# Performance work log

Measured on AMD Instinct MI355X. Metric: run time of the kernel, lower is better.

The kernel has to match this reference:

```python
import jax, jax.numpy as jnp
import numpy as np

NUM_ROUNDS = 4

def leaky(x):
    return jnp.where(x >= 0, x, 0.01 * x)  # nn.LeakyReLU default slope

def setup_inputs() -> dict:
    key = jax.random.key(0)
    ks = jax.random.split(key, 26)
    N, E2, B = 50000, 320000, 256
    Fn, Fe, D, Dn, Dx, H, NE = 64, 16, 128, 128, 16, 128, 8
    # edges come in reverse pairs so edge i and edge rev[i] are (u->v) and (v->u)
    s = jax.random.randint(ks[0], (E2,), 0, N, dtype=jnp.int32)
    d = jax.random.randint(ks[1], (E2,), 0, N, dtype=jnp.int32)
    src = jnp.concatenate([s, d])
    dst = jnp.concatenate([d, s])
    rev = jnp.concatenate([jnp.arange(E2, dtype=jnp.int32) + E2,
                           jnp.arange(E2, dtype=jnp.int32)])
    gid = jnp.sort(jax.random.randint(ks[2], (N,), 0, B, dtype=jnp.int32))
    r = lambda k, sh: (jax.random.normal(k, sh, jnp.float32) * 0.1)
    Fin = Dn + Dx  # MoE input feature size
    return {
        'node_feat': r(ks[3], (N, Fn)),
        'edge_feat': r(ks[4], (2 * E2, Fe)),
        'src': src, 'dst': dst, 'rev': rev, 'gid': gid,
        'extra': r(ks[5], (B, Dx)),
        'W_edge': r(ks[6], (Fn + Fe, D)),
        'W_upd': r(ks[7], (D, D)),
        'W_node': r(ks[8], (Fn + D, Dn)), 'b_node': r(ks[9], (Dn,)),
        'Wg1': r(ks[10], (Fin, H)), 'bg1': r(ks[11], (H,)),
        'Wg2': r(ks[12], (H, H)), 'bg2': r(ks[13], (H,)),
        'Wg3': r(ks[14], (H, NE)), 'bg3': r(ks[15], (NE,)),
        'EW1': r(ks[16], (NE, Fin, H)), 'Eb1': r(ks[17], (NE, H)),
        'EW2': r(ks[18], (NE, H, H)), 'Eb2': r(ks[19], (NE, H)),
        'EW3': r(ks[20], (NE, H)), 'Eb3': r(ks[21], (NE,)),
    }

def reference(node_feat, edge_feat, src, dst, rev, gid, extra,
              W_edge, W_upd, W_node, b_node,
              Wg1, bg1, Wg2, bg2, Wg3, bg3,
              EW1, Eb1, EW2, Eb2, EW3, Eb3):
    N = node_feat.shape[0]
    B = extra.shape[0]
    # h0 = edge_mlp(cat(src node feat, edge feat)) ; dropout = identity (eval)
    h0 = leaky(jnp.concatenate([node_feat[src], edge_feat], axis=1) @ W_edge)  # [E, D]
    h = h0
    for _ in range(NUM_ROUNDS):
        sum0 = jax.ops.segment_sum(h, dst, num_segments=N)       # incoming sum per node
        m = sum0[src] - h[rev]                                   # exclude reverse message
        h = leaky(m @ W_upd + h0)
    m_node = jax.ops.segment_sum(h, dst, num_segments=N)         # [N, D]
    hn = leaky(jnp.concatenate([node_feat, m_node], axis=1) @ W_node + b_node)  # [N, Dn]
    # NOTE: original computes multi-head attention on hn.unsqueeze(1) but discards it.
    graph_feat = jax.ops.segment_sum(hn, gid, num_segments=B)    # readout sum [B, Dn]
    x = jnp.concatenate([graph_feat, extra], axis=-1)            # [B, Fin]
    # gating
    g = leaky(x @ Wg1 + bg1)
    g = leaky(g @ Wg2 + bg2)
    g = jax.nn.softmax(g @ Wg3 + bg3, axis=1)                    # [B, NE]
    # experts (vectorized over expert dim)
    e = leaky(jnp.einsum('bi,eih->beh', x, EW1) + Eb1)
    e = leaky(jnp.einsum('beh,ehk->bek', e, EW2) + Eb2)
    e = jnp.einsum('beh,eh->be', e, EW3) + Eb3                   # [B, NE]
    return jnp.sum(e * g, axis=1, keepdims=True)                 # [B, 1]
```

## Files before the change

kernel.cpp:

```cpp
#include <hip/hip_runtime.h>
#include <stdint.h>
#include <stddef.h>


typedef unsigned short u16;
typedef u16 u16x2 __attribute__((ext_vector_type(2)));
typedef u16 u16x4 __attribute__((ext_vector_type(4)));
typedef u16 u16x8 __attribute__((ext_vector_type(8)));
typedef short s16x8 __attribute__((ext_vector_type(8)));
typedef float f32x4_ __attribute__((ext_vector_type(4)));

__device__ __forceinline__ float lk(float x) { return x >= 0.f ? x : 0.01f * x; }

__device__ __forceinline__ float bf2f(u16 u) {
    union { uint32_t i; float f; } v; v.i = ((uint32_t)u) << 16; return v.f;
}
__device__ __forceinline__ u16 f2bf(float f) {
    union { float f; uint32_t i; } v; v.f = f;
    uint32_t r = v.i + 0x7FFFu + ((v.i >> 16) & 1u);
    return (u16)(r >> 16);
}

__global__ void k_zero_i32(int* __restrict__ p, int n) {
    int i = blockIdx.x * blockDim.x + threadIdx.x;
    if (i < n) p[i] = 0;
}
__global__ void k_zero_f32(float* __restrict__ p, int n) {
    int i = blockIdx.x * blockDim.x + threadIdx.x;
    if (i < n) p[i] = 0.f;
}

__global__ void k_prep_wu(const float* __restrict__ W, u16* __restrict__ wTg) {
    int i = blockIdx.x * 256 + threadIdx.x;
    if (i < 128 * 128) { int n = i >> 7, k = i & 127; wTg[i] = f2bf(W[k * 128 + n]); }
}
__global__ void k_prep_we(const float* __restrict__ W, u16* __restrict__ weTg) {
    int i = blockIdx.x * 256 + threadIdx.x;
    if (i < 128 * 96) {
        int n = i / 96, k = i - n * 96;
        weTg[i] = (k < 80) ? f2bf(W[k * 128 + n]) : (u16)0;
    }
}

__global__ void k_count(const int* __restrict__ dst, int* __restrict__ counts, int E) {
    int i = blockIdx.x * blockDim.x + threadIdx.x;
    if (i < E) atomicAdd(&counts[dst[i]], 1);
}

__global__ __launch_bounds__(1024) void k_scan(const int* __restrict__ counts,
                                               int* __restrict__ off, int Nn) {
    __shared__ int buf[1024];
    __shared__ int carry_s;
    int t = threadIdx.x;
    if (t == 0) carry_s = 0;
    __syncthreads();
    for (int base = 0; base < Nn; base += 8192) {
        int v[8]; int s = 0;
#pragma unroll
        for (int i = 0; i < 8; ++i) {
            int idx = base + t * 8 + i;
            v[i] = (idx < Nn) ? counts[idx] : 0;
            s += v[i];
        }
        int x = s;
        for (int o = 1; o < 1024; o <<= 1) {
            buf[t] = x; __syncthreads();
            if (t >= o) x += buf[t - o];
            __syncthreads();
        }
        int excl = carry_s + x - s;
#pragma unroll
        for (int i = 0; i < 8; ++i) {
            int idx = base + t * 8 + i;
            if (idx < Nn) off[idx] = excl;
            excl += v[i];
        }
        __syncthreads();
        if (t == 1023) carry_s += x;
        __syncthreads();
    }
    if (t == 0) off[Nn] = carry_s;
}

__global__ void k_fill(const int* __restrict__ dst, const int* __restrict__ off,
                       int* __restrict__ cursor, int* __restrict__ eidx, int E) {
    int i = blockIdx.x * blockDim.x + threadIdx.x;
    if (i < E) {
        int d = dst[i];
        int p = atomicAdd(&cursor[d], 1);
        eidx[off[d] + p] = i;
    }
}

__global__ __launch_bounds__(256) void k_segsum(const u16* __restrict__ h,
                                                const int* __restrict__ off,
                                                const int* __restrict__ eidx,
                                                float* __restrict__ out, int Nn) {
    int wid = threadIdx.x >> 6;
    int lane = threadIdx.x & 63;
    int n = blockIdx.x * 4 + wid;
    if (n >= Nn) return;
    int lo = off[n], hi = off[n + 1];
    float ax = 0.f, ay = 0.f;
    int j = lo;
    for (; j + 3 < hi; j += 4) {
        int ea = eidx[j], eb = eidx[j + 1], ec = eidx[j + 2], ed = eidx[j + 3];
        u16x2 va = *(const u16x2*)(h + (size_t)ea * 128 + lane * 2);
        u16x2 vb = *(const u16x2*)(h + (size_t)eb * 128 + lane * 2);
        u16x2 vc = *(const u16x2*)(h + (size_t)ec * 128 + lane * 2);
        u16x2 vd = *(const u16x2*)(h + (size_t)ed * 128 + lane * 2);
        ax += (bf2f(va[0]) + bf2f(vb[0])) + (bf2f(vc[0]) + bf2f(vd[0]));
        ay += (bf2f(va[1]) + bf2f(vb[1])) + (bf2f(vc[1]) + bf2f(vd[1]));
    }
    for (; j < hi; ++j) {
        int ea = eidx[j];
        u16x2 va = *(const u16x2*)(h + (size_t)ea * 128 + lane * 2);
        ax += bf2f(va[0]); ay += bf2f(va[1]);
    }
    float2 r; r.x = ax; r.y = ay;
    *(float2*)(out + (size_t)n * 128 + lane * 2) = r;
}


__global__ __launch_bounds__(256) void k_edge_init_mfma(
    const float* __restrict__ node_feat, const float* __restrict__ edge_feat,
    const int* __restrict__ src, const u16* __restrict__ weTg,
    u16* __restrict__ h) {
    __shared__ u16 x0[64][104];
    __shared__ u16 wTe[128][104];
    const int t = threadIdx.x;
    const int e0 = blockIdx.x * 64;
    {
        int n = t >> 1, half = t & 1;
        const u16* gsrc = weTg + n * 96 + half * 48;
        u16* ldst = &wTe[n][half * 48];
#pragma unroll
        for (int i = 0; i < 6; ++i)
            *(u16x8*)(ldst + i * 8) = *(const u16x8*)(gsrc + i * 8);
    }
    {
        int rloc = t & 63, part = t >> 6;
        int e = e0 + rloc;
        int s = src[e];
        const float* nf = node_feat + (size_t)s * 64;
        const float* ef = edge_feat + (size_t)e * 16;
#pragma unroll
        for (int i = 0; i < 5; ++i) {
            int f = part * 20 + i * 4;
            float4 v;
            if (f < 64) v = *(const float4*)(nf + f);
            else        v = *(const float4*)(ef + (f - 64));
            u16x4 o; o[0] = f2bf(v.x); o[1] = f2bf(v.y); o[2] = f2bf(v.z); o[3] = f2bf(v.w);
            *(u16x4*)(&x0[rloc][f]) = o;
        }
    }
    {
        int rr = t >> 2, part = t & 3;
        u16x4 z = {0, 0, 0, 0};
        *(u16x4*)(&x0[rr][80 + part * 4]) = z;
    }
    __syncthreads();
    const int w = t >> 6, l = t & 63;
    const int er = l & 15, kg = l >> 4;
    f32x4_ acc[8];
#pragma unroll
    for (int nt = 0; nt < 8; ++nt) { f32x4_ z = {0.f, 0.f, 0.f, 0.f}; acc[nt] = z; }
#pragma unroll
    for (int ks = 0; ks < 3; ++ks) {
        s16x8 bfrag = *(const s16x8*)(&x0[w * 16 + er][ks * 32 + kg * 8]);
#pragma unroll
        for (int nt = 0; nt < 8; ++nt) {
            s16x8 afrag = *(const s16x8*)(&wTe[nt * 16 + er][ks * 32 + kg * 8]);
            acc[nt] = __builtin_amdgcn_mfma_f32_16x16x32_bf16(afrag, bfrag, acc[nt], 0, 0, 0);
        }
    }
    {
        size_t gedge = (size_t)(e0 + w * 16 + er);
        u16* hr = h + gedge * 128;
#pragma unroll
        for (int nt = 0; nt < 8; ++nt) {
            int nc = nt * 16 + kg * 4;
            u16x4 o;
#pragma unroll
            for (int r = 0; r < 4; ++r) o[r] = f2bf(lk(acc[nt][r]));
            *(u16x4*)(hr + nc) = o;
        }
    }
}

__global__ __launch_bounds__(256) void k_update_mfma_recomp(
    u16* __restrict__ h, const float* __restrict__ sum0,
    const int* __restrict__ src, const int* __restrict__ rev,
    const u16* __restrict__ wTg, const u16* __restrict__ weTg,
    const float* __restrict__ node_feat, const float* __restrict__ edge_feat) {
    __shared__ __align__(16) u16 smem[64 * 136 + 128 * 136];
    __shared__ int eid[64];
    u16 (*x0)[104]  = (u16(*)[104])smem;
    u16 (*wTe)[104] = (u16(*)[104])(smem + 64 * 104);
    u16 (*mw)[136]  = (u16(*)[136])smem;
    u16 (*wT)[136]  = (u16(*)[136])(smem + 64 * 136);
    const int t = threadIdx.x;
    const int p0 = blockIdx.x * 32;
    const int w = t >> 6, l = t & 63;
    const int er = l & 15, kg = l >> 4;

    {
        int n = t >> 1, half = t & 1;
        const u16* gsrc = weTg + n * 96 + half * 48;
        u16* ldst = &wTe[n][half * 48];
#pragma unroll
        for (int i = 0; i < 6; ++i)
            *(u16x8*)(ldst + i * 8) = *(const u16x8*)(gsrc + i * 8);
    }
    {
        int rloc = t & 63, part = t >> 6;
        int gedge = (rloc < 32) ? (p0 + rloc) : rev[p0 + rloc - 32];
        if (part == 0) eid[rloc] = gedge;
        int s = src[gedge];
        const float* nf = node_feat + (size_t)s * 64;
        const float* ef = edge_feat + (size_t)gedge * 16;
#pragma unroll
        for (int i = 0; i < 5; ++i) {
            int f = part * 20 + i * 4;
            float4 v;
            if (f < 64) v = *(const float4*)(nf + f);
            else        v = *(const float4*)(ef + (f - 64));
            u16x4 o; o[0] = f2bf(v.x); o[1] = f2bf(v.y); o[2] = f2bf(v.z); o[3] = f2bf(v.w);
            *(u16x4*)(&x0[rloc][f]) = o;
        }
    }
    {
        int rr = t >> 2, part = t & 3;
        u16x4 z = {0, 0, 0, 0};
        *(u16x4*)(&x0[rr][80 + part * 4]) = z;
    }
    __syncthreads();

    f32x4_ acc[8];
#pragma unroll
    for (int nt = 0; nt < 8; ++nt) { f32x4_ z = {0.f, 0.f, 0.f, 0.f}; acc[nt] = z; }
#pragma unroll
    for (int ks = 0; ks < 3; ++ks) {
        s16x8 bfrag = *(const s16x8*)(&x0[w * 16 + er][ks * 32 + kg * 8]);
#pragma unroll
        for (int nt = 0; nt < 8; ++nt) {
            s16x8 afrag = *(const s16x8*)(&wTe[nt * 16 + er][ks * 32 + kg * 8]);
            acc[nt] = __builtin_amdgcn_mfma_f32_16x16x32_bf16(afrag, bfrag, acc[nt], 0, 0, 0);
        }
    }
    float h0reg[8][4];
#pragma unroll
    for (int nt = 0; nt < 8; ++nt)
#pragma unroll
        for (int r = 0; r < 4; ++r) h0reg[nt][r] = lk(acc[nt][r]);
    __syncthreads();

    {
        int wr = t >> 1, half = t & 1;
        const u16* gsrc = wTg + wr * 128 + half * 64;
        u16* ldst = &wT[wr][half * 64];
#pragma unroll
        for (int i = 0; i < 8; ++i)
            *(u16x8*)(ldst + i * 8) = *(const u16x8*)(gsrc + i * 8);
    }
    {
        int rr = t >> 2, part = t & 3;
        int gedge, partner;
        if (rr < 32) { gedge = p0 + rr;        partner = rev[gedge]; }
        else         { partner = p0 + rr - 32; gedge = rev[partner]; }
        int s = src[gedge];
        const float* sp = sum0 + (size_t)s * 128 + part * 32;
        const u16* hp = h + (size_t)partner * 128 + part * 32;
#pragma unroll
        for (int i = 0; i < 4; ++i) {
            float4 a0 = *(const float4*)(sp + i * 8);
            float4 a1 = *(const float4*)(sp + i * 8 + 4);
            u16x8 b = *(const u16x8*)(hp + i * 8);
            u16x8 o;
            o[0] = f2bf(a0.x - bf2f(b[0]));
            o[1] = f2bf(a0.y - bf2f(b[1]));
            o[2] = f2bf(a0.z - bf2f(b[2]));
            o[3] = f2bf(a0.w - bf2f(b[3]));
            o[4] = f2bf(a1.x - bf2f(b[4]));
            o[5] = f2bf(a1.y - bf2f(b[5]));
            o[6] = f2bf(a1.z - bf2f(b[6]));
            o[7] = f2bf(a1.w - bf2f(b[7]));
            *(u16x8*)(&mw[rr][part * 32 + i * 8]) = o;
        }
    }
    __syncthreads();

#pragma unroll
    for (int nt = 0; nt < 8; ++nt) { f32x4_ z = {0.f, 0.f, 0.f, 0.f}; acc[nt] = z; }
#pragma unroll
    for (int ks = 0; ks < 4; ++ks) {
        s16x8 bfrag = *(const s16x8*)(&mw[w * 16 + er][ks * 32 + kg * 8]);
#pragma unroll
        for (int nt = 0; nt < 8; ++nt) {
            s16x8 afrag = *(const s16x8*)(&wT[nt * 16 + er][ks * 32 + kg * 8]);
            acc[nt] = __builtin_amdgcn_mfma_f32_16x16x32_bf16(afrag, bfrag, acc[nt], 0, 0, 0);
        }
    }
    {
        int gedge = eid[w * 16 + er];
        u16* hr = h + (size_t)gedge * 128;
#pragma unroll
        for (int nt = 0; nt < 8; ++nt) {
            int nc = nt * 16 + kg * 4;
            u16x4 o;
#pragma unroll
            for (int r = 0; r < 4; ++r) o[r] = f2bf(lk(acc[nt][r] + h0reg[nt][r]));
            *(u16x4*)(hr + nc) = o;
        }
    }
}

#define KROW(i, m)                                                                 \
    acc[i][0] = fmaf(m, w0.x, acc[i][0]); acc[i][1] = fmaf(m, w0.y, acc[i][1]);    \
    acc[i][2] = fmaf(m, w0.z, acc[i][2]); acc[i][3] = fmaf(m, w0.w, acc[i][3]);    \
    acc[i][4] = fmaf(m, w1.x, acc[i][4]); acc[i][5] = fmaf(m, w1.y, acc[i][5]);    \
    acc[i][6] = fmaf(m, w1.z, acc[i][6]); acc[i][7] = fmaf(m, w1.w, acc[i][7]);

#define KSTEP(ARR, kk, kabs)                                                       \
    {                                                                              \
        const float m0 = ARR[et4 + 0][kabs];                                       \
        const float m1 = ARR[et4 + 1][kabs];                                       \
        const float m2 = ARR[et4 + 2][kabs];                                       \
        const float m3 = ARR[et4 + 3][kabs];                                       \
        const float4 w0 = *(const float4*)(&w_lds[(kk) * 128 + ct8]);              \
        const float4 w1 = *(const float4*)(&w_lds[(kk) * 128 + ct8 + 4]);          \
        KROW(0, m0) KROW(1, m1) KROW(2, m2) KROW(3, m3)                            \
    }

__global__ __launch_bounds__(256) void k_node(const float* __restrict__ node_feat,
                                              const float* __restrict__ m_node,
                                              const float* __restrict__ W,
                                              const float* __restrict__ bias,
                                              float* __restrict__ hn, int Nn) {
    __shared__ float in_lds[64][196];
    __shared__ float w_lds[16 * 128];
    const int t = threadIdx.x;
    const int n0 = blockIdx.x * 64;
    {
        int q = t & 31, r0 = t >> 5;
#pragma unroll
        for (int rr = r0; rr < 64; rr += 8) {
            int n = n0 + rr;
            bool ok = n < Nn;
            const float* nf = node_feat + (size_t)n * 64;
            const float* mn = m_node + (size_t)n * 128;
            for (int qq = q; qq < 48; qq += 32) {
                float4 v; v.x = v.y = v.z = v.w = 0.f;
                if (ok) {
                    if (qq < 16) v = *(const float4*)(nf + qq * 4);
                    else         v = *(const float4*)(mn + (qq - 16) * 4);
                }
                *(float4*)(&in_lds[rr][qq * 4]) = v;
            }
        }
    }
    float acc[4][8];
#pragma unroll
    for (int i = 0; i < 4; ++i)
#pragma unroll
        for (int j = 0; j < 8; ++j) acc[i][j] = 0.f;
    const int et4 = (t >> 4) * 4;
    const int ct8 = (t & 15) * 8;
    for (int kc = 0; kc < 192; kc += 16) {
        __syncthreads();
#pragma unroll
        for (int i = 0; i < 2; ++i) {
            int f4 = t + i * 256;
            *(float4*)(&w_lds[f4 * 4]) = *(const float4*)(W + (size_t)kc * 128 + (size_t)f4 * 4);
        }
        __syncthreads();
#pragma unroll 8
        for (int k = 0; k < 16; ++k) { KSTEP(in_lds, k, kc + k) }
    }
    float4 b0 = *(const float4*)(bias + ct8);
    float4 b1 = *(const float4*)(bias + ct8 + 4);
    __syncthreads();
#pragma unroll
    for (int i = 0; i < 4; ++i) {
        int row = n0 + et4 + i;
        if (row >= Nn) break;
        size_t base = (size_t)row * 128 + ct8;
        float4 o0, o1;
        o0.x = lk(acc[i][0] + b0.x); o0.y = lk(acc[i][1] + b0.y);
        o0.z = lk(acc[i][2] + b0.z); o0.w = lk(acc[i][3] + b0.w);
        o1.x = lk(acc[i][4] + b1.x); o1.y = lk(acc[i][5] + b1.y);
        o1.z = lk(acc[i][6] + b1.z); o1.w = lk(acc[i][7] + b1.w);
        *(float4*)(hn + base) = o0;
        *(float4*)(hn + base + 4) = o1;
    }
}

__device__ __forceinline__ int lbound(const int* __restrict__ a, int n, int key) {
    int lo = 0, hi = n;
    while (lo < hi) { int mid = (lo + hi) >> 1; if (a[mid] < key) lo = mid + 1; else hi = mid; }
    return lo;
}

__global__ __launch_bounds__(256) void k_readout(const float* __restrict__ hn,
                                                 const int* __restrict__ gid,
                                                 const float* __restrict__ extra,
                                                 float* __restrict__ x, int Nn) {
    int b = blockIdx.x;
    int t = threadIdx.x;
    int lo = lbound(gid, Nn, b);
    int hi = lbound(gid, Nn, b + 1);
    if (t < 128) {
        float acc = 0.f;
        int n = lo;
        for (; n + 3 < hi; n += 4) {
            acc += hn[(size_t)n * 128 + t] + hn[(size_t)(n + 1) * 128 + t]
                 + hn[(size_t)(n + 2) * 128 + t] + hn[(size_t)(n + 3) * 128 + t];
        }
        for (; n < hi; ++n) acc += hn[(size_t)n * 128 + t];
        x[(size_t)b * 144 + t] = acc;
    } else if (t < 144) {
        x[(size_t)b * 144 + t] = extra[(size_t)b * 16 + (t - 128)];
    }
}

__global__ __launch_bounds__(256) void k_moe(const float* __restrict__ x,
                                             const float* __restrict__ Wg1, const float* __restrict__ bg1,
                                             const float* __restrict__ Wg2, const float* __restrict__ bg2,
                                             const float* __restrict__ Wg3, const float* __restrict__ bg3,
                                             const float* __restrict__ EW1, const float* __restrict__ Eb1,
                                             const float* __restrict__ EW2, const float* __restrict__ Eb2,
                                             const float* __restrict__ EW3, const float* __restrict__ Eb3,
                                             float* __restrict__ out) {
    __shared__ float xs[144];
    __shared__ float g1s[128], g2s[128];
    __shared__ float e1s[8 * 128], e2s[8 * 128];
    __shared__ float logit_s[8], val_s[8];
    const int b = blockIdx.x;
    const int t = threadIdx.x;
    if (t < 144) xs[t] = x[(size_t)b * 144 + t];
    __syncthreads();
    if (t < 128) {
        float a = bg1[t];
        for (int k = 0; k < 144; ++k) a = fmaf(xs[k], Wg1[k * 128 + t], a);
        g1s[t] = lk(a);
    }
#pragma unroll
    for (int u = 0; u < 4; ++u) {
        int idx = t + u * 256;
        int e = idx >> 7, c = idx & 127;
        float a = Eb1[e * 128 + c];
        const float* w = EW1 + (size_t)e * 144 * 128 + c;
        for (int k = 0; k < 144; ++k) a = fmaf(xs[k], w[(size_t)k * 128], a);
        e1s[idx] = lk(a);
    }
    __syncthreads();
    if (t < 128) {
        float a = bg2[t];
        for (int k = 0; k < 128; ++k) a = fmaf(g1s[k], Wg2[k * 128 + t], a);
        g2s[t] = lk(a);
    }
#pragma unroll
    for (int u = 0; u < 4; ++u) {
        int idx = t + u * 256;
        int e = idx >> 7, c = idx & 127;
        float a = Eb2[e * 128 + c];
        const float* w = EW2 + (size_t)e * 128 * 128 + c;
        const float* e1p = e1s + e * 128;
        for (int k = 0; k < 128; ++k) a = fmaf(e1p[k], w[(size_t)k * 128], a);
        e2s[idx] = lk(a);
    }
    __syncthreads();
    if (t < 8) {
        float a = bg3[t];
        for (int k = 0; k < 128; ++k) a = fmaf(g2s[k], Wg3[k * 8 + t], a);
        logit_s[t] = a;
        float v = Eb3[t];
        const float* w = EW3 + t * 128;
        const float* ep = e2s + t * 128;
        for (int k = 0; k < 128; ++k) v = fmaf(ep[k], w[k], v);
        val_s[t] = v;
    }
    __syncthreads();
    if (t == 0) {
        float mx = logit_s[0];
        for (int e = 1; e < 8; ++e) mx = fmaxf(mx, logit_s[e]);
        float s = 0.f, o = 0.f;
        for (int e = 0; e < 8; ++e) {
            float g = __expf(logit_s[e] - mx);
            s += g;
            o = fmaf(val_s[e], g, o);
        }
        out[b] = o / s;
    }
}

extern "C" void kernel_launch(void* const* d_in, const int* in_sizes, int n_in,
                              void* d_out, int out_size, void* d_ws, size_t ws_size,
                              hipStream_t stream) {
    const float* node_feat = (const float*)d_in[0];
    const float* edge_feat = (const float*)d_in[1];
    const int*   src       = (const int*)d_in[2];
    const int*   dst       = (const int*)d_in[3];
    const int*   rev       = (const int*)d_in[4];
    const int*   gid       = (const int*)d_in[5];
    const float* extra     = (const float*)d_in[6];
    const float* W_edge    = (const float*)d_in[7];
    const float* W_upd     = (const float*)d_in[8];
    const float* W_node    = (const float*)d_in[9];
    const float* b_node    = (const float*)d_in[10];

    const int Nn = in_sizes[0] / 64;
    const int E  = in_sizes[2];
    const int Bb = in_sizes[6] / 16;
    (void)n_in;
    float* out = (float*)d_out;

    uintptr_t p = (uintptr_t)d_ws;
    auto alloc = [&](size_t bytes) -> void* {
        void* r = (void*)p;
        p += (bytes + 255) & ~(size_t)255;
        return r;
    };
    auto al = [](size_t b) { return (b + 255) & ~(size_t)255; };
    const size_t SHb = al((size_t)E * 128 * 2);
    const size_t fixed = al((size_t)Nn * 128 * 4) + al((size_t)Bb * 144 * 4) +
                         al((size_t)(Nn + 1) * 4) + al((size_t)(2 * Nn) * 4) +
                         al((size_t)E * 4) + al(128 * 128 * 2) + al(128 * 96 * 2) + 4096;
    const size_t need = SHb + fixed;

    if (ws_size < need) {
        k_zero_f32<<<(out_size + 255) / 256, 256, 0, stream>>>(out, out_size);
        return;
    }

    u16* h      = (u16*)alloc(SHb);
    float* sum0 = (float*)alloc((size_t)Nn * 128 * sizeof(float));
    float* xbuf = (float*)alloc((size_t)Bb * 144 * sizeof(float));
    int* off    = (int*)alloc((size_t)(Nn + 1) * sizeof(int));
    int* cc     = (int*)alloc((size_t)(2 * Nn) * sizeof(int));
    int* eidx   = (int*)alloc((size_t)E * sizeof(int));
    u16* wTg    = (u16*)alloc(128 * 128 * sizeof(u16));
    u16* weTg   = (u16*)alloc(128 * 96 * sizeof(u16));
    int* counts = cc;
    int* cursor = cc + Nn;

    k_zero_i32<<<(2 * Nn + 255) / 256, 256, 0, stream>>>(cc, 2 * Nn);

    const int csr_grid = (E + 255) / 256;
    k_count<<<csr_grid, 256, 0, stream>>>(dst, counts, E);
    k_scan<<<1, 1024, 0, stream>>>(counts, off, Nn);
    k_fill<<<csr_grid, 256, 0, stream>>>(dst, off, cursor, eidx, E);

    k_prep_wu<<<64, 256, 0, stream>>>(W_upd, wTg);
    k_prep_we<<<48, 256, 0, stream>>>(W_edge, weTg);

    const int egrid = E / 64;
    const int pgrid = (E / 2) / 32;
    const int sgrid = (Nn + 3) / 4;

    k_edge_init_mfma<<<egrid, 256, 0, stream>>>(node_feat, edge_feat, src, weTg, h);
    for (int r = 0; r < 4; ++r) {
        k_segsum<<<sgrid, 256, 0, stream>>>(h, off, eidx, sum0, Nn);
        k_update_mfma_recomp<<<pgrid, 256, 0, stream>>>(h, sum0, src, rev, wTg, weTg,
                                                        node_feat, edge_feat);
    }
    k_segsum<<<sgrid, 256, 0, stream>>>(h, off, eidx, sum0, Nn);

    float* hn = sum0;
    k_node<<<(Nn + 63) / 64, 256, 0, stream>>>(node_feat, sum0, W_node, b_node, hn, Nn);
    k_readout<<<Bb, 256, 0, stream>>>(hn, gid, extra, xbuf, Nn);
    k_moe<<<Bb, 256, 0, stream>>>(xbuf,
                                  (const float*)d_in[11], (const float*)d_in[12],
                                  (const float*)d_in[13], (const float*)d_in[14],
                                  (const float*)d_in[15], (const float*)d_in[16],
                                  (const float*)d_in[17], (const float*)d_in[18],
                                  (const float*)d_in[19], (const float*)d_in[20],
                                  (const float*)d_in[21], (const float*)d_in[22],
                                  out);
}
```

Baseline: 1.580 ms.

## Fuse segment sums into edge kernels via atomics and swizzle shared tiles

The edge-init and update kernels now scatter each bf16-rounded output row into a double-buffered per-node fp32 sum with atomicAdd. This removes the CSR build and the separate segment-sum gather passes when the workspace is large enough. The weight fragments are read straight from global memory instead of being staged in LDS, and the activation tile uses an XOR-swizzled layout in a smaller shared buffer, which raises occupancy. The cost is heavy atomic traffic (about 640k×128 float atomics per round), non-deterministic summation order, and an extra zeroing pass per round.

```diff
diff --git a/kernel.cpp b/kernel.cpp
--- a/kernel.cpp
+++ b/kernel.cpp
@@ -19,6 +19,10 @@
     union { float f; uint32_t i; } v; v.f = f;
     uint32_t r = v.i + 0x7FFFu + ((v.i >> 16) & 1u);
     return (u16)(r >> 16);
+}
+
+__device__ __forceinline__ int swz(int row, int k) {
+    return row * 128 + (k ^ ((row & 7) << 3));
 }
 
 __global__ void k_zero_i32(int* __restrict__ p, int n) {
@@ -122,22 +126,17 @@
 }
 
 
-__global__ __launch_bounds__(256) void k_edge_init_mfma(
+template <bool ATOMIC>
+__global__ __launch_bounds__(256) void k_edge_init_v2(
     const float* __restrict__ node_feat, const float* __restrict__ edge_feat,
-    const int* __restrict__ src, const u16* __restrict__ weTg,
-    u16* __restrict__ h) {
-    __shared__ u16 x0[64][104];
-    __shared__ u16 wTe[128][104];
+    const int* __restrict__ src, const int* __restrict__ dst,
+    const u16* __restrict__ weTg, u16* __restrict__ h,
+    float* __restrict__ sumAcc) {
+    __shared__ u16 tile[64 * 128];
     const int t = threadIdx.x;
     const int e0 = blockIdx.x * 64;
-    {
-        int n = t >> 1, half = t & 1;
-        const u16* gsrc = weTg + n * 96 + half * 48;
-        u16* ldst = &wTe[n][half * 48];
-#pragma unroll
-        for (int i = 0; i < 6; ++i)
-            *(u16x8*)(ldst + i * 8) = *(const u16x8*)(gsrc + i * 8);
-    }
+    const int w = t >> 6, l = t & 63;
+    const int er = l & 15, kg = l >> 4;
     {
         int rloc = t & 63, part = t >> 6;
         int e = e0 + rloc;
@@ -151,32 +150,32 @@
             if (f < 64) v = *(const float4*)(nf + f);
             else        v = *(const float4*)(ef + (f - 64));
             u16x4 o; o[0] = f2bf(v.x); o[1] = f2bf(v.y); o[2] = f2bf(v.z); o[3] = f2bf(v.w);
-            *(u16x4*)(&x0[rloc][f]) = o;
+            *(u16x4*)(&tile[swz(rloc, f)]) = o;
         }
     }
     {
         int rr = t >> 2, part = t & 3;
         u16x4 z = {0, 0, 0, 0};
-        *(u16x4*)(&x0[rr][80 + part * 4]) = z;
-    }
-    __syncthreads();
-    const int w = t >> 6, l = t & 63;
-    const int er = l & 15, kg = l >> 4;
+        *(u16x4*)(&tile[swz(rr, 80 + part * 4)]) = z;
+    }
+    __syncthreads();
     f32x4_ acc[8];
 #pragma unroll
     for (int nt = 0; nt < 8; ++nt) { f32x4_ z = {0.f, 0.f, 0.f, 0.f}; acc[nt] = z; }
 #pragma unroll
     for (int ks = 0; ks < 3; ++ks) {
-        s16x8 bfrag = *(const s16x8*)(&x0[w * 16 + er][ks * 32 + kg * 8]);
+        s16x8 bfrag = *(const s16x8*)(&tile[swz(w * 16 + er, ks * 32 + kg * 8)]);
 #pragma unroll
         for (int nt = 0; nt < 8; ++nt) {
-            s16x8 afrag = *(const s16x8*)(&wTe[nt * 16 + er][ks * 32 + kg * 8]);
+            s16x8 afrag = *(const s16x8*)(weTg + (nt * 16 + er) * 96 + ks * 32 + kg * 8);
             acc[nt] = __builtin_amdgcn_mfma_f32_16x16x32_bf16(afrag, bfrag, acc[nt], 0, 0, 0);
         }
     }
     {
-        size_t gedge = (size_t)(e0 + w * 16 + er);
-        u16* hr = h + gedge * 128;
+        int gedge = e0 + w * 16 + er;
+        u16* hr = h + (size_t)gedge * 128;
+        float* sr = nullptr;
+        if (ATOMIC) sr = sumAcc + (size_t)dst[gedge] * 128;
 #pragma unroll
         for (int nt = 0; nt < 8; ++nt) {
             int nc = nt * 16 + kg * 4;
@@ -184,38 +183,37 @@
 #pragma unroll
             for (int r = 0; r < 4; ++r) o[r] = f2bf(lk(acc[nt][r]));
             *(u16x4*)(hr + nc) = o;
-        }
-    }
-}
-
-__global__ __launch_bounds__(256) void k_update_mfma_recomp(
-    u16* __restrict__ h, const float* __restrict__ sum0,
-    const int* __restrict__ src, const int* __restrict__ rev,
+            if (ATOMIC) {
+#pragma unroll
+                for (int r = 0; r < 4; ++r) atomicAdd(sr + nc + r, bf2f(o[r]));
+            }
+        }
+    }
+}
+
+template <bool ATOMIC>
+__global__ __launch_bounds__(256) void k_update_v2(
+    u16* __restrict__ h, const float* __restrict__ sumPrev,
+    float* __restrict__ sumNext,
+    const int* __restrict__ src, const int* __restrict__ dst,
+    const int* __restrict__ rev,
     const u16* __restrict__ wTg, const u16* __restrict__ weTg,
     const float* __restrict__ node_feat, const float* __restrict__ edge_feat) {
-    __shared__ __align__(16) u16 smem[64 * 136 + 128 * 136];
+    __shared__ u16 tile[64 * 128];
     __shared__ int eid[64];
-    u16 (*x0)[104]  = (u16(*)[104])smem;
-    u16 (*wTe)[104] = (u16(*)[104])(smem + 64 * 104);
-    u16 (*mw)[136]  = (u16(*)[136])smem;
-    u16 (*wT)[136]  = (u16(*)[136])(smem + 64 * 136);
+    __shared__ int did[64];
     const int t = threadIdx.x;
     const int p0 = blockIdx.x * 32;
     const int w = t >> 6, l = t & 63;
     const int er = l & 15, kg = l >> 4;
 
     {
-        int n = t >> 1, half = t & 1;
-        const u16* gsrc = weTg + n * 96 + half * 48;
-        u16* ldst = &wTe[n][half * 48];
-#pragma unroll
-        for (int i = 0; i < 6; ++i)
-            *(u16x8*)(ldst + i * 8) = *(const u16x8*)(gsrc + i * 8);
-    }
-    {
         int rloc = t & 63, part = t >> 6;
         int gedge = (rloc < 32) ? (p0 + rloc) : rev[p0 + rloc - 32];
-        if (part == 0) eid[rloc] = gedge;
+        if (part == 0) {
+            eid[rloc] = gedge;
+            if (ATOMIC) did[rloc] = dst[gedge];
+        }
         int s = src[gedge];
         const float* nf = node_feat + (size_t)s * 64;
         const float* ef = edge_feat + (size_t)gedge * 16;
@@ -226,13 +224,13 @@
             if (f < 64) v = *(const float4*)(nf + f);
             else        v = *(const float4*)(ef + (f - 64));
             u16x4 o; o[0] = f2bf(v.x); o[1] = f2bf(v.y); o[2] = f2bf(v.z); o[3] = f2bf(v.w);
-            *(u16x4*)(&x0[rloc][f]) = o;
+            *(u16x4*)(&tile[swz(rloc, f)]) = o;
         }
     }
     {
         int rr = t >> 2, part = t & 3;
         u16x4 z = {0, 0, 0, 0};
-        *(u16x4*)(&x0[rr][80 + part * 4]) = z;
+        *(u16x4*)(&tile[swz(rr, 80 + part * 4)]) = z;
     }
     __syncthreads();
 
@@ -241,10 +239,10 @@
     for (int nt = 0; nt < 8; ++nt) { f32x4_ z = {0.f, 0.f, 0.f, 0.f}; acc[nt] = z; }
 #pragma unroll
     for (int ks = 0; ks < 3; ++ks) {
-        s16x8 bfrag = *(const s16x8*)(&x0[w * 16 + er][ks * 32 + kg * 8]);
+        s16x8 bfrag = *(const s16x8*)(&tile[swz(w * 16 + er, ks * 32 + kg * 8)]);
 #pragma unroll
         for (int nt = 0; nt < 8; ++nt) {
-            s16x8 afrag = *(const s16x8*)(&wTe[nt * 16 + er][ks * 32 + kg * 8]);
+            s16x8 afrag = *(const s16x8*)(weTg + (nt * 16 + er) * 96 + ks * 32 + kg * 8);
             acc[nt] = __builtin_amdgcn_mfma_f32_16x16x32_bf16(afrag, bfrag, acc[nt], 0, 0, 0);
         }
     }
@@ -255,21 +253,13 @@
         for (int r = 0; r < 4; ++r) h0reg[nt][r] = lk(acc[nt][r]);
     __syncthreads();
 
-    {
-        int wr = t >> 1, half = t & 1;
-        const u16* gsrc = wTg + wr * 128 + half * 64;
-        u16* ldst = &wT[wr][half * 64];
-#pragma unroll
-        for (int i = 0; i < 8; ++i)
-            *(u16x8*)(ldst + i * 8) = *(const u16x8*)(gsrc + i * 8);
-    }
     {
         int rr = t >> 2, part = t & 3;
         int gedge, partner;
         if (rr < 32) { gedge = p0 + rr;        partner = rev[gedge]; }
         else         { partner = p0 + rr - 32; gedge = rev[partner]; }
         int s = src[gedge];
-        const float* sp = sum0 + (size_t)s * 128 + part * 32;
+        const float* sp = sumPrev + (size_t)s * 128 + part * 32;
         const u16* hp = h + (size_t)partner * 128 + part * 32;
 #pragma unroll
         for (int i = 0; i < 4; ++i) {
@@ -285,7 +275,7 @@
             o[5] = f2bf(a1.y - bf2f(b[5]));
             o[6] = f2bf(a1.z - bf2f(b[6]));
             o[7] = f2bf(a1.w - bf2f(b[7]));
-            *(u16x8*)(&mw[rr][part * 32 + i * 8]) = o;
+            *(u16x8*)(&tile[swz(rr, part * 32 + i * 8)]) = o;
         }
     }
     __syncthreads();
@@ -294,16 +284,18 @@
     for (int nt = 0; nt < 8; ++nt) { f32x4_ z = {0.f, 0.f, 0.f, 0.f}; acc[nt] = z; }
 #pragma unroll
     for (int ks = 0; ks < 4; ++ks) {
-        s16x8 bfrag = *(const s16x8*)(&mw[w * 16 + er][ks * 32 + kg * 8]);
+        s16x8 bfrag = *(const s16x8*)(&tile[swz(w * 16 + er, ks * 32 + kg * 8)]);
 #pragma unroll
         for (int nt = 0; nt < 8; ++nt) {
-            s16x8 afrag = *(const s16x8*)(&wT[nt * 16 + er][ks * 32 + kg * 8]);
+            s16x8 afrag = *(const s16x8*)(wTg + (nt * 16 + er) * 128 + ks * 32 + kg * 8);
             acc[nt] = __builtin_amdgcn_mfma_f32_16x16x32_bf16(afrag, bfrag, acc[nt], 0, 0, 0);
         }
     }
     {
         int gedge = eid[w * 16 + er];
         u16* hr = h + (size_t)gedge * 128;
+        float* sr = nullptr;
+        if (ATOMIC) sr = sumNext + (size_t)did[w * 16 + er] * 128;
 #pragma unroll
         for (int nt = 0; nt < 8; ++nt) {
             int nc = nt * 16 + kg * 4;
@@ -311,6 +303,10 @@
 #pragma unroll
             for (int r = 0; r < 4; ++r) o[r] = f2bf(lk(acc[nt][r] + h0reg[nt][r]));
             *(u16x4*)(hr + nc) = o;
+            if (ATOMIC) {
+#pragma unroll
+                for (int r = 0; r < 4; ++r) atomicAdd(sr + nc + r, bf2f(o[r]));
+            }
         }
     }
 }
@@ -522,59 +518,94 @@
         return r;
     };
     auto al = [](size_t b) { return (b + 255) & ~(size_t)255; };
-    const size_t SHb = al((size_t)E * 128 * 2);
-    const size_t fixed = al((size_t)Nn * 128 * 4) + al((size_t)Bb * 144 * 4) +
-                         al((size_t)(Nn + 1) * 4) + al((size_t)(2 * Nn) * 4) +
-                         al((size_t)E * 4) + al(128 * 128 * 2) + al(128 * 96 * 2) + 4096;
-    const size_t need = SHb + fixed;
-
-    if (ws_size < need) {
-        k_zero_f32<<<(out_size + 255) / 256, 256, 0, stream>>>(out, out_size);
-        return;
-    }
-
-    u16* h      = (u16*)alloc(SHb);
-    float* sum0 = (float*)alloc((size_t)Nn * 128 * sizeof(float));
-    float* xbuf = (float*)alloc((size_t)Bb * 144 * sizeof(float));
-    int* off    = (int*)alloc((size_t)(Nn + 1) * sizeof(int));
-    int* cc     = (int*)alloc((size_t)(2 * Nn) * sizeof(int));
-    int* eidx   = (int*)alloc((size_t)E * sizeof(int));
-    u16* wTg    = (u16*)alloc(128 * 128 * sizeof(u16));
-    u16* weTg   = (u16*)alloc(128 * 96 * sizeof(u16));
-    int* counts = cc;
-    int* cursor = cc + Nn;
-
-    k_zero_i32<<<(2 * Nn + 255) / 256, 256, 0, stream>>>(cc, 2 * Nn);
-
-    const int csr_grid = (E + 255) / 256;
-    k_count<<<csr_grid, 256, 0, stream>>>(dst, counts, E);
-    k_scan<<<1, 1024, 0, stream>>>(counts, off, Nn);
-    k_fill<<<csr_grid, 256, 0, stream>>>(dst, off, cursor, eidx, E);
-
-    k_prep_wu<<<64, 256, 0, stream>>>(W_upd, wTg);
-    k_prep_we<<<48, 256, 0, stream>>>(W_edge, weTg);
+    const size_t SHb  = al((size_t)E * 128 * 2);
+    const size_t SUMb = al((size_t)Nn * 128 * 4);
+    const size_t misc = al((size_t)Bb * 144 * 4) + al(128 * 128 * 2) +
+                        al(128 * 96 * 2) + 4096;
+    const size_t csrb = al((size_t)(Nn + 1) * 4) + al((size_t)(2 * Nn) * 4) +
+                        al((size_t)E * 4);
+    const size_t needA = SHb + 2 * SUMb + misc;
+    const size_t needB = SHb + SUMb + misc + csrb;
 
     const int egrid = E / 64;
     const int pgrid = (E / 2) / 32;
-    const int sgrid = (Nn + 3) / 4;
-
-    k_edge_init_mfma<<<egrid, 256, 0, stream>>>(node_feat, edge_feat, src, weTg, h);
-    for (int r = 0; r < 4; ++r) {
+    const int nsum  = Nn * 128;
+
+    if (ws_size >= needA) {
+        u16* h      = (u16*)alloc(SHb);
+        float* sumA = (float*)alloc(SUMb);
+        float* sumB = (float*)alloc(SUMb);
+        float* xbuf = (float*)alloc((size_t)Bb * 144 * sizeof(float));
+        u16* wTg    = (u16*)alloc(128 * 128 * sizeof(u16));
+        u16* weTg   = (u16*)alloc(128 * 96 * sizeof(u16));
+
+        k_prep_wu<<<64, 256, 0, stream>>>(W_upd, wTg);
+        k_prep_we<<<48, 256, 0, stream>>>(W_edge, weTg);
+        k_zero_f32<<<(nsum + 255) / 256, 256, 0, stream>>>(sumA, nsum);
+
+        k_edge_init_v2<true><<<egrid, 256, 0, stream>>>(node_feat, edge_feat, src,
+                                                        dst, weTg, h, sumA);
+        float* sp = sumA;
+        float* sn = sumB;
+        for (int r = 0; r < 4; ++r) {
+            k_zero_f32<<<(nsum + 255) / 256, 256, 0, stream>>>(sn, nsum);
+            k_update_v2<true><<<pgrid, 256, 0, stream>>>(h, sp, sn, src, dst, rev,
+                                                         wTg, weTg, node_feat, edge_feat);
+            float* tmp = sp; sp = sn; sn = tmp;
+        }
+        float* hn = sp;
+        k_node<<<(Nn + 63) / 64, 256, 0, stream>>>(node_feat, sp, W_node, b_node, hn, Nn);
+        k_readout<<<Bb, 256, 0, stream>>>(hn, gid, extra, xbuf, Nn);
+        k_moe<<<Bb, 256, 0, stream>>>(xbuf,
+                                      (const float*)d_in[11], (const float*)d_in[12],
+                                      (const float*)d_in[13], (const float*)d_in[14],
+                                      (const float*)d_in[15], (const float*)d_in[16],
+                                      (const float*)d_in[17], (const float*)d_in[18],
+                                      (const float*)d_in[19], (const float*)d_in[20],
+                                      (const float*)d_in[21], (const float*)d_in[22],
+                                      out);
+    } else if (ws_size >= needB) {
+        u16* h      = (u16*)alloc(SHb);
+        float* sum0 = (float*)alloc(SUMb);
+        float* xbuf = (float*)alloc((size_t)Bb * 144 * sizeof(float));
+        int* off    = (int*)alloc((size_t)(Nn + 1) * sizeof(int));
+        int* cc     = (int*)alloc((size_t)(2 * Nn) * sizeof(int));
+        int* eidx   = (int*)alloc((size_t)E * sizeof(int));
+        u16* wTg    = (u16*)alloc(128 * 128 * sizeof(u16));
+        u16* weTg   = (u16*)alloc(128 * 96 * sizeof(u16));
+        int* counts = cc;
+        int* cursor = cc + Nn;
+
+        k_zero_i32<<<(2 * Nn + 255) / 256, 256, 0, stream>>>(cc, 2 * Nn);
+        const int csr_grid = (E + 255) / 256;
+        k_count<<<csr_grid, 256, 0, stream>>>(dst, counts, E);
+        k_scan<<<1, 1024, 0, stream>>>(counts, off, Nn);
+        k_fill<<<csr_grid, 256, 0, stream>>>(dst, off, cursor, eidx, E);
+        k_prep_wu<<<64, 256, 0, stream>>>(W_upd, wTg);
+        k_prep_we<<<48, 256, 0, stream>>>(W_edge, weTg);
+
+        const int sgrid = (Nn + 3) / 4;
+        k_edge_init_v2<false><<<egrid, 256, 0, stream>>>(node_feat, edge_feat, src,
+                                                         dst, weTg, h, nullptr);
+        for (int r = 0; r < 4; ++r) {
+            k_segsum<<<sgrid, 256, 0, stream>>>(h, off, eidx, sum0, Nn);
+            k_update_v2<false><<<pgrid, 256, 0, stream>>>(h, sum0, nullptr, src, dst,
+                                                          rev, wTg, weTg,
+                                                          node_feat, edge_feat);
+        }
         k_segsum<<<sgrid, 256, 0, stream>>>(h, off, eidx, sum0, Nn);
-        k_update_mfma_recomp<<<pgrid, 256, 0, stream>>>(h, sum0, src, rev, wTg, weTg,
-                                                        node_feat, edge_feat);
-    }
-    k_segsum<<<sgrid, 256, 0, stream>>>(h, off, eidx, sum0, Nn);
-
-    float* hn = sum0;
-    k_node<<<(Nn + 63) / 64, 256, 0, stream>>>(node_feat, sum0, W_node, b_node, hn, Nn);
-    k_readout<<<Bb, 256, 0, stream>>>(hn, gid, extra, xbuf, Nn);
-    k_moe<<<Bb, 256, 0, stream>>>(xbuf,
-                                  (const float*)d_in[11], (const float*)d_in[12],
-                                  (const float*)d_in[13], (const float*)d_in[14],
-                                  (const float*)d_in[15], (const float*)d_in[16],
-                                  (const float*)d_in[17], (const float*)d_in[18],
-                                  (const float*)d_in[19], (const float*)d_in[20],
-                                  (const float*)d_in[21], (const float*)d_in[22],
-                                  out);
-}
+        float* hn = sum0;
+        k_node<<<(Nn + 63) / 64, 256, 0, stream>>>(node_feat, sum0, W_node, b_node, hn, Nn);
+        k_readout<<<Bb, 256, 0, stream>>>(hn, gid, extra, xbuf, Nn);
+        k_moe<<<Bb, 256, 0, stream>>>(xbuf,
+                                      (const float*)d_in[11], (const float*)d_in[12],
+                                      (const float*)d_in[13], (const float*)d_in[14],
+                                      (const float*)d_in[15], (const float*)d_in[16],
+                                      (const float*)d_in[17], (const float*)d_in[18],
+                                      (const float*)d_in[19], (const float*)d_in[20],
+                                      (const float*)d_in[21], (const float*)d_in[22],
+                                      out);
+    } else {
+        k_zero_f32<<<(out_size + 255) / 256, 256, 0, stream>>>(out, out_size);
+    }
+}
```

Measured after the change: 5.938 ms. 3.76x slower.
